# Optimization experiments

Hardware: AMD Instinct MI355X
Metric: run time of the kernel (lower is better)

The kernel has to match this reference:

```python
import jax, jax.numpy as jnp
import numpy as np

IN_F = 4096
OUT_F = 4096
ROWS = 8192  # batch*seq


def setup_inputs() -> dict:
    key = jax.random.key(0)
    k1, k2, k3 = jax.random.split(key, 3)
    scale = (2.0 / IN_F) ** 0.5
    x = jax.random.normal(k1, (ROWS, IN_F), dtype=jnp.float32)
    weight_real = jax.random.normal(k2, (OUT_F, IN_F), dtype=jnp.float32) * scale
    weight_imag = jax.random.normal(k3, (OUT_F, IN_F), dtype=jnp.float32) * scale
    bias = jnp.zeros((OUT_F,), dtype=jnp.float32)
    return {"x": x, "weight_real": weight_real, "weight_imag": weight_imag, "bias": bias}


def reference(x, weight_real, weight_imag, bias):
    # complex matmul with real input x: out_c = x @ (Wr + i Wi)^T
    real = jnp.matmul(x, weight_real.T)   # [rows, out]
    imag = jnp.matmul(x, weight_imag.T)   # [rows, out]
    magnitude = jnp.sqrt(real * real + imag * imag)  # torch.abs(out_c)
    phase = jnp.arctan2(imag, real)                   # torch.angle(out_c)
    interference = jnp.cos(phase)
    return magnitude * interference + bias
```

## Files before the change

### kernel.cpp

```cpp
#include <hip/hip_runtime.h>
#include <hip/hip_bf16.h>
#include <cstdint>
#include <cstddef>


#define TILE 128
#define BK 64

typedef short bf16x8 __attribute__((ext_vector_type(8)));
typedef float f32x4 __attribute__((ext_vector_type(4)));

__device__ __forceinline__ unsigned short f2bf(float f) {
  unsigned int x = __float_as_uint(f);
  unsigned int r = x + 0x7FFFu + ((x >> 16) & 1u);
  return (unsigned short)(r >> 16);
}

__global__ void cvt_both_f32_to_bf16(const float* __restrict__ x,
                                     const float* __restrict__ wr,
                                     unsigned short* __restrict__ xa,
                                     unsigned short* __restrict__ wb,
                                     int nA8, int nB8) {
  int i = blockIdx.x * blockDim.x + threadIdx.x;
  int stride = gridDim.x * blockDim.x;
  int total = nA8 + nB8;
  for (; i < total; i += stride) {
    const float* src; unsigned short* dst; int j;
    if (i < nA8) { src = x;  dst = xa; j = i; }
    else         { src = wr; dst = wb; j = i - nA8; }
    float4 a = ((const float4*)src)[2 * j];
    float4 b = ((const float4*)src)[2 * j + 1];
    union { unsigned short u[8]; uint4 v; } o;
    o.u[0] = f2bf(a.x); o.u[1] = f2bf(a.y);
    o.u[2] = f2bf(a.z); o.u[3] = f2bf(a.w);
    o.u[4] = f2bf(b.x); o.u[5] = f2bf(b.y);
    o.u[6] = f2bf(b.z); o.u[7] = f2bf(b.w);
    ((uint4*)dst)[j] = o.v;
  }
}

template <bool DIRECT>
__global__ void gemm_bt_bf16(const unsigned short* __restrict__ Abf,
                             const unsigned short* __restrict__ Bbf,
                             const float* __restrict__ Afp,
                             const float* __restrict__ Bfp,
                             const float* __restrict__ bias,
                             float* __restrict__ C,
                             int M, int N, int K) {
  __shared__ unsigned short Als[TILE * BK];
  __shared__ unsigned short Bls[TILE * BK];

  const int tid = threadIdx.x;
  const int wave = tid >> 6;
  const int lane = tid & 63;
  const int lrow = lane & 15;
  const int quad = lane >> 4;
  const int mW = (wave >> 1) * 64;
  const int nW = (wave & 1) * 64;
  const int row0 = blockIdx.y * TILE;
  const int col0 = blockIdx.x * TILE;

  f32x4 acc[4][4];
  const f32x4 zero = {0.f, 0.f, 0.f, 0.f};
#pragma unroll
  for (int i = 0; i < 4; ++i)
#pragma unroll
    for (int j = 0; j < 4; ++j) acc[i][j] = zero;

  for (int k0 = 0; k0 < K; k0 += BK) {
    if (DIRECT) {
#pragma unroll
      for (int c = 0; c < 4; ++c) {
        int e = c * 256 + tid;
        int r = e >> 3;
        int kc = (e & 7) * 8;
        const unsigned short* ga = Abf + (size_t)(row0 + r) * K + k0 + kc;
        const unsigned short* gb = Bbf + (size_t)(col0 + r) * K + k0 + kc;
        unsigned short* la = Als + (size_t)(c * 256 + wave * 64) * 8;
        unsigned short* lb = Bls + (size_t)(c * 256 + wave * 64) * 8;
        __builtin_amdgcn_global_load_lds(
            (const __attribute__((address_space(1))) void*)ga,
            (__attribute__((address_space(3))) void*)la, 16, 0, 0);
        __builtin_amdgcn_global_load_lds(
            (const __attribute__((address_space(1))) void*)gb,
            (__attribute__((address_space(3))) void*)lb, 16, 0, 0);
      }
    } else {
#pragma unroll
      for (int c = 0; c < 4; ++c) {
        int e0 = (c * 256 + tid) * 8;
        int r = e0 >> 6;
        int kc = e0 & 63;
        const float* ga = Afp + (size_t)(row0 + r) * K + k0 + kc;
        const float* gb = Bfp + (size_t)(col0 + r) * K + k0 + kc;
        float4 a0 = ((const float4*)ga)[0];
        float4 a1 = ((const float4*)ga)[1];
        float4 b0 = ((const float4*)gb)[0];
        float4 b1 = ((const float4*)gb)[1];
        union { unsigned short u[8]; uint4 v; } oa, ob;
        oa.u[0] = f2bf(a0.x); oa.u[1] = f2bf(a0.y);
        oa.u[2] = f2bf(a0.z); oa.u[3] = f2bf(a0.w);
        oa.u[4] = f2bf(a1.x); oa.u[5] = f2bf(a1.y);
        oa.u[6] = f2bf(a1.z); oa.u[7] = f2bf(a1.w);
        ob.u[0] = f2bf(b0.x); ob.u[1] = f2bf(b0.y);
        ob.u[2] = f2bf(b0.z); ob.u[3] = f2bf(b0.w);
        ob.u[4] = f2bf(b1.x); ob.u[5] = f2bf(b1.y);
        ob.u[6] = f2bf(b1.z); ob.u[7] = f2bf(b1.w);
        *(uint4*)&Als[e0] = oa.v;
        *(uint4*)&Bls[e0] = ob.v;
      }
    }
    __syncthreads();

#pragma unroll
    for (int h = 0; h < 2; ++h) {
      bf16x8 af[4], bfr[4];
#pragma unroll
      for (int t = 0; t < 4; ++t) {
        af[t]  = *(const bf16x8*)&Als[(mW + t * 16 + lrow) * BK + h * 32 + quad * 8];
        bfr[t] = *(const bf16x8*)&Bls[(nW + t * 16 + lrow) * BK + h * 32 + quad * 8];
      }
#pragma unroll
      for (int mt = 0; mt < 4; ++mt)
#pragma unroll
        for (int nt = 0; nt < 4; ++nt)
          acc[mt][nt] = __builtin_amdgcn_mfma_f32_16x16x32_bf16(
              af[mt], bfr[nt], acc[mt][nt], 0, 0, 0);
    }
    __syncthreads();
  }

#pragma unroll
  for (int nt = 0; nt < 4; ++nt) {
    int col = col0 + nW + nt * 16 + lrow;
    float bv = bias[col];
#pragma unroll
    for (int mt = 0; mt < 4; ++mt) {
      int rowb = row0 + mW + mt * 16 + quad * 4;
#pragma unroll
      for (int r = 0; r < 4; ++r) {
        C[(size_t)(rowb + r) * N + col] = acc[mt][nt][r] + bv;
      }
    }
  }
}

extern "C" void kernel_launch(void* const* d_in, const int* in_sizes, int n_in,
                              void* d_out, int out_size, void* d_ws, size_t ws_size,
                              hipStream_t stream) {
  const int M = 8192, N = 4096, K = 4096;
  const float* x = (const float*)d_in[0];
  const float* wr = (const float*)d_in[1];
  const float* bias = (const float*)d_in[3];
  float* out = (float*)d_out;

  const size_t nA = (size_t)M * K;
  const size_t nB = (size_t)N * K;
  dim3 grid(N / TILE, M / TILE);

  if (ws_size >= (nA + nB) * sizeof(unsigned short)) {
    unsigned short* xa = (unsigned short*)d_ws;
    unsigned short* wb = xa + nA;
    hipLaunchKernelGGL(cvt_both_f32_to_bf16, dim3(4096), dim3(256), 0, stream,
                       x, wr, xa, wb, (int)(nA / 8), (int)(nB / 8));
    hipLaunchKernelGGL((gemm_bt_bf16<true>), grid, dim3(256), 0, stream,
                       xa, wb, (const float*)nullptr, (const float*)nullptr,
                       bias, out, M, N, K);
  } else {
    hipLaunchKernelGGL((gemm_bt_bf16<false>), grid, dim3(256), 0, stream,
                       (const unsigned short*)nullptr, (const unsigned short*)nullptr,
                       x, wr, bias, out, M, N, K);
  }
}
```

Before: 577.1 us.

## Replace LDS-staged GEMM with register-streamed direct global loads and swapped grid

The bf16 GEMM path drops LDS staging and barriers. Each wave now loads its MFMA fragments straight from global memory into registers, double-buffered across two 32-wide K halves, with launch bounds set for three blocks per CU. The grid is also transposed so consecutive blocks walk along M, which changes L2 reuse of the weight tiles. The cost removed is the LDS writes, reads and syncs. In exchange there is no sharing of tiles between waves, so global/L2 traffic is higher and the strided 16-byte row loads are poorly coalesced.

```diff
diff --git a/kernel.cpp b/kernel.cpp
--- a/kernel.cpp
+++ b/kernel.cpp
@@ -5,7 +5,7 @@
 
 
 #define TILE 128
-#define BK 64
+#define KD 4096
 
 typedef short bf16x8 __attribute__((ext_vector_type(8)));
 typedef float f32x4 __attribute__((ext_vector_type(4)));
@@ -39,17 +39,89 @@
   }
 }
 
-template <bool DIRECT>
-__global__ void gemm_bt_bf16(const unsigned short* __restrict__ Abf,
-                             const unsigned short* __restrict__ Bbf,
-                             const float* __restrict__ Afp,
-                             const float* __restrict__ Bfp,
-                             const float* __restrict__ bias,
-                             float* __restrict__ C,
-                             int M, int N, int K) {
-  __shared__ unsigned short Als[TILE * BK];
-  __shared__ unsigned short Bls[TILE * BK];
-
+__global__ __launch_bounds__(256, 3)
+void gemm_stream_bf16(const unsigned short* __restrict__ A,
+                      const unsigned short* __restrict__ B,
+                      const float* __restrict__ bias,
+                      float* __restrict__ C, int M, int N) {
+  const int tid = threadIdx.x;
+  const int wave = tid >> 6;
+  const int lane = tid & 63;
+  const int lrow = lane & 15;
+  const int quad = lane >> 4;
+  const int mW = (wave >> 1) * 64;
+  const int nW = (wave & 1) * 64;
+  const int row0 = blockIdx.x * TILE;
+  const int col0 = blockIdx.y * TILE;
+
+  const unsigned short* aP = A + (size_t)(row0 + mW + lrow) * KD + quad * 8;
+  const unsigned short* bP = B + (size_t)(col0 + nW + lrow) * KD + quad * 8;
+
+  f32x4 acc[4][4];
+  const f32x4 zero = {0.f, 0.f, 0.f, 0.f};
+#pragma unroll
+  for (int i = 0; i < 4; ++i)
+#pragma unroll
+    for (int j = 0; j < 4; ++j) acc[i][j] = zero;
+
+  bf16x8 a0[4], b0[4], a1[4], b1[4];
+#pragma unroll
+  for (int t = 0; t < 4; ++t) {
+    a0[t] = *(const bf16x8*)(aP + (size_t)t * 16 * KD);
+    b0[t] = *(const bf16x8*)(bP + (size_t)t * 16 * KD);
+  }
+
+  for (int k0 = 0; k0 < KD; k0 += 64) {
+#pragma unroll
+    for (int t = 0; t < 4; ++t) {
+      a1[t] = *(const bf16x8*)(aP + (size_t)t * 16 * KD + k0 + 32);
+      b1[t] = *(const bf16x8*)(bP + (size_t)t * 16 * KD + k0 + 32);
+    }
+#pragma unroll
+    for (int mt = 0; mt < 4; ++mt)
+#pragma unroll
+      for (int nt = 0; nt < 4; ++nt)
+        acc[mt][nt] = __builtin_amdgcn_mfma_f32_16x16x32_bf16(
+            a0[mt], b0[nt], acc[mt][nt], 0, 0, 0);
+
+    if (k0 + 64 < KD) {
+#pragma unroll
+      for (int t = 0; t < 4; ++t) {
+        a0[t] = *(const bf16x8*)(aP + (size_t)t * 16 * KD + k0 + 64);
+        b0[t] = *(const bf16x8*)(bP + (size_t)t * 16 * KD + k0 + 64);
+      }
+    }
+#pragma unroll
+    for (int mt = 0; mt < 4; ++mt)
+#pragma unroll
+      for (int nt = 0; nt < 4; ++nt)
+        acc[mt][nt] = __builtin_amdgcn_mfma_f32_16x16x32_bf16(
+            a1[mt], b1[nt], acc[mt][nt], 0, 0, 0);
+  }
+
+#pragma unroll
+  for (int nt = 0; nt < 4; ++nt) {
+    int col = col0 + nW + nt * 16 + lrow;
+    float bv = bias[col];
+#pragma unroll
+    for (int mt = 0; mt < 4; ++mt) {
+      int rowb = row0 + mW + mt * 16 + quad * 4;
+#pragma unroll
+      for (int r = 0; r < 4; ++r) {
+        C[(size_t)(rowb + r) * N + col] = acc[mt][nt][r] + bv;
+      }
+    }
+  }
+}
+
+#define BKF 32
+__global__ void gemm_bt_f32in(const float* __restrict__ Afp,
+                              const float* __restrict__ Bfp,
+                              const float* __restrict__ bias,
+                              float* __restrict__ C,
+                              int M, int N, int K) {
+  __shared__ unsigned short Als[TILE * BKF];
+  __shared__ unsigned short Bls[TILE * BKF];
   const int tid = threadIdx.x;
   const int wave = tid >> 6;
   const int lane = tid & 63;
@@ -67,69 +139,45 @@
 #pragma unroll
     for (int j = 0; j < 4; ++j) acc[i][j] = zero;
 
-  for (int k0 = 0; k0 < K; k0 += BK) {
-    if (DIRECT) {
-#pragma unroll
-      for (int c = 0; c < 4; ++c) {
-        int e = c * 256 + tid;
-        int r = e >> 3;
-        int kc = (e & 7) * 8;
-        const unsigned short* ga = Abf + (size_t)(row0 + r) * K + k0 + kc;
-        const unsigned short* gb = Bbf + (size_t)(col0 + r) * K + k0 + kc;
-        unsigned short* la = Als + (size_t)(c * 256 + wave * 64) * 8;
-        unsigned short* lb = Bls + (size_t)(c * 256 + wave * 64) * 8;
-        __builtin_amdgcn_global_load_lds(
-            (const __attribute__((address_space(1))) void*)ga,
-            (__attribute__((address_space(3))) void*)la, 16, 0, 0);
-        __builtin_amdgcn_global_load_lds(
-            (const __attribute__((address_space(1))) void*)gb,
-            (__attribute__((address_space(3))) void*)lb, 16, 0, 0);
-      }
-    } else {
-#pragma unroll
-      for (int c = 0; c < 4; ++c) {
-        int e0 = (c * 256 + tid) * 8;
-        int r = e0 >> 6;
-        int kc = e0 & 63;
-        const float* ga = Afp + (size_t)(row0 + r) * K + k0 + kc;
-        const float* gb = Bfp + (size_t)(col0 + r) * K + k0 + kc;
-        float4 a0 = ((const float4*)ga)[0];
-        float4 a1 = ((const float4*)ga)[1];
-        float4 b0 = ((const float4*)gb)[0];
-        float4 b1 = ((const float4*)gb)[1];
-        union { unsigned short u[8]; uint4 v; } oa, ob;
-        oa.u[0] = f2bf(a0.x); oa.u[1] = f2bf(a0.y);
-        oa.u[2] = f2bf(a0.z); oa.u[3] = f2bf(a0.w);
-        oa.u[4] = f2bf(a1.x); oa.u[5] = f2bf(a1.y);
-        oa.u[6] = f2bf(a1.z); oa.u[7] = f2bf(a1.w);
-        ob.u[0] = f2bf(b0.x); ob.u[1] = f2bf(b0.y);
-        ob.u[2] = f2bf(b0.z); ob.u[3] = f2bf(b0.w);
-        ob.u[4] = f2bf(b1.x); ob.u[5] = f2bf(b1.y);
-        ob.u[6] = f2bf(b1.z); ob.u[7] = f2bf(b1.w);
-        *(uint4*)&Als[e0] = oa.v;
-        *(uint4*)&Bls[e0] = ob.v;
-      }
+  for (int k0 = 0; k0 < K; k0 += BKF) {
+#pragma unroll
+    for (int c = 0; c < 2; ++c) {
+      int e0 = c * 2048 + tid * 8;
+      int r = e0 >> 5;
+      int kc = e0 & 31;
+      const float* ga = Afp + (size_t)(row0 + r) * K + k0 + kc;
+      const float* gb = Bfp + (size_t)(col0 + r) * K + k0 + kc;
+      float4 af0 = ((const float4*)ga)[0];
+      float4 af1 = ((const float4*)ga)[1];
+      float4 bf0 = ((const float4*)gb)[0];
+      float4 bf1 = ((const float4*)gb)[1];
+      union { unsigned short u[8]; uint4 v; } oa, ob;
+      oa.u[0] = f2bf(af0.x); oa.u[1] = f2bf(af0.y);
+      oa.u[2] = f2bf(af0.z); oa.u[3] = f2bf(af0.w);
+      oa.u[4] = f2bf(af1.x); oa.u[5] = f2bf(af1.y);
+      oa.u[6] = f2bf(af1.z); oa.u[7] = f2bf(af1.w);
+      ob.u[0] = f2bf(bf0.x); ob.u[1] = f2bf(bf0.y);
+      ob.u[2] = f2bf(bf0.z); ob.u[3] = f2bf(bf0.w);
+      ob.u[4] = f2bf(bf1.x); ob.u[5] = f2bf(bf1.y);
+      ob.u[6] = f2bf(bf1.z); ob.u[7] = f2bf(bf1.w);
+      *(uint4*)&Als[e0] = oa.v;
+      *(uint4*)&Bls[e0] = ob.v;
     }
     __syncthreads();
-
-#pragma unroll
-    for (int h = 0; h < 2; ++h) {
-      bf16x8 af[4], bfr[4];
-#pragma unroll
-      for (int t = 0; t < 4; ++t) {
-        af[t]  = *(const bf16x8*)&Als[(mW + t * 16 + lrow) * BK + h * 32 + quad * 8];
-        bfr[t] = *(const bf16x8*)&Bls[(nW + t * 16 + lrow) * BK + h * 32 + quad * 8];
-      }
-#pragma unroll
-      for (int mt = 0; mt < 4; ++mt)
-#pragma unroll
-        for (int nt = 0; nt < 4; ++nt)
-          acc[mt][nt] = __builtin_amdgcn_mfma_f32_16x16x32_bf16(
-              af[mt], bfr[nt], acc[mt][nt], 0, 0, 0);
-    }
+    bf16x8 af[4], bfr[4];
+#pragma unroll
+    for (int t = 0; t < 4; ++t) {
+      af[t]  = *(const bf16x8*)&Als[(mW + t * 16 + lrow) * BKF + quad * 8];
+      bfr[t] = *(const bf16x8*)&Bls[(nW + t * 16 + lrow) * BKF + quad * 8];
+    }
+#pragma unroll
+    for (int mt = 0; mt < 4; ++mt)
+#pragma unroll
+      for (int nt = 0; nt < 4; ++nt)
+        acc[mt][nt] = __builtin_amdgcn_mfma_f32_16x16x32_bf16(
+            af[mt], bfr[nt], acc[mt][nt], 0, 0, 0);
     __syncthreads();
   }
-
 #pragma unroll
   for (int nt = 0; nt < 4; ++nt) {
     int col = col0 + nW + nt * 16 + lrow;
@@ -156,19 +204,18 @@
 
   const size_t nA = (size_t)M * K;
   const size_t nB = (size_t)N * K;
-  dim3 grid(N / TILE, M / TILE);
 
   if (ws_size >= (nA + nB) * sizeof(unsigned short)) {
     unsigned short* xa = (unsigned short*)d_ws;
     unsigned short* wb = xa + nA;
     hipLaunchKernelGGL(cvt_both_f32_to_bf16, dim3(4096), dim3(256), 0, stream,
                        x, wr, xa, wb, (int)(nA / 8), (int)(nB / 8));
-    hipLaunchKernelGGL((gemm_bt_bf16<true>), grid, dim3(256), 0, stream,
-                       xa, wb, (const float*)nullptr, (const float*)nullptr,
-                       bias, out, M, N, K);
+    dim3 grid(M / TILE, N / TILE);
+    hipLaunchKernelGGL(gemm_stream_bf16, grid, dim3(256), 0, stream,
+                       xa, wb, bias, out, M, N);
   } else {
-    hipLaunchKernelGGL((gemm_bt_bf16<false>), grid, dim3(256), 0, stream,
-                       (const unsigned short*)nullptr, (const unsigned short*)nullptr,
+    dim3 grid(N / TILE, M / TILE);
+    hipLaunchKernelGGL(gemm_bt_f32in, grid, dim3(256), 0, stream,
                        x, wr, bias, out, M, N, K);
   }
 }
```

After: 1.193 ms. +106.7%, slower.
